# Kernel tuning notes

Hardware: AMD Instinct MI355X
Metric: run time of the kernel (lower is better)

## Reference

```python
import jax, jax.numpy as jnp
import numpy as np

POOLSCALE = 4  # HSA: avg-pool kernel/stride = (scale, scale*4)

def _avg_pool(x, kh, kw):
    # kernel == stride and dims divisible -> exact reshape-mean pooling
    B, C, H, W = x.shape
    return x.reshape(B, C, H // kh, kh, W // kw, kw).mean(axis=(3, 5))

def setup_inputs() -> dict:
    key = jax.random.key(0)
    k1, k2, k3 = jax.random.split(key, 3)
    shape = (4, 64, 192, 192)
    return {
        "K": jax.random.normal(k1, shape, dtype=jnp.float32),
        "Q": jax.random.normal(k2, shape, dtype=jnp.float32),
        "V": jax.random.normal(k3, shape, dtype=jnp.float32),
    }

def reference(K, Q, V):
    B, C, H, W = Q.shape
    kh, kw = POOLSCALE, POOLSCALE * 4
    Qp = Q.reshape(B, C, H * W).transpose(0, 2, 1)          # [B, HW, C]
    Kp = _avg_pool(K, kh, kw)                               # [B, C, h, w]
    Kp = Kp.reshape(B, C, -1)                               # [B, C, hw_p]
    Vp = _avg_pool(V, kh, kw).reshape(B, C, -1)             # [B, C, hw_p]
    scores = jnp.einsum('bnc,bcm->bnm', Qp, Kp)             # [B, HW, hw_p]
    attn = jax.nn.softmax(scores, axis=1)                   # softmax over query dim (dim=1), as in torch code
    out = jnp.einsum('bcm,bnm->bcn', Vp, attn)              # V_pie @ attn^T -> [B, C, HW]
    return out.reshape(B, C, H, W)
```

## Files before the change

kernel.cpp:

```cpp
#include <hip/hip_runtime.h>
#include <stdint.h>

#define BB 4
#define CC 64
#define HH 192
#define WW 192
#define HWN (HH*WW)
#define KH 4
#define KW 16
#define PW (WW/KW)
#define MP ((HH/KH)*(WW/KW))
#define MITER (MP/64)
#define NCHUNK (HWN/256)
#define SCALE_W 65536.0f
#define INV_SCALE (1.0f/65536.0f)

typedef _Float16 half8 __attribute__((ext_vector_type(8)));
typedef _Float16 half4 __attribute__((ext_vector_type(4)));
typedef float floatx4 __attribute__((ext_vector_type(4)));

static __device__ __forceinline__ void gload16(const void* g, void* l) {
  __builtin_amdgcn_global_load_lds((const __attribute__((address_space(1))) void*)g,
                                   (__attribute__((address_space(3))) void*)l, 16, 0, 0);
}
#define WAITCNT_VM(N) asm volatile("s_waitcnt vmcnt(" #N ")" ::: "memory")
#define WAITCNT_LGKM0 asm volatile("s_waitcnt lgkmcnt(0)" ::: "memory")


__global__ __launch_bounds__(256) void pool_kernel(
    const float* __restrict__ Kin, const float* __restrict__ Vin,
    _Float16* __restrict__ kptF, float* __restrict__ vp) {
  int t = blockIdx.x * 256 + threadIdx.x;
  const int total = BB * CC * MP;
  bool isV = t >= total;
  int idx = isV ? t - total : t;
  int m = idx % MP;
  int c = (idx / MP) % CC;
  int b = idx / (MP * CC);
  int mh = m / PW, mw = m % PW;
  const float* src = (isV ? Vin : Kin) + (((b * CC + c) * HH + mh * KH) * WW + mw * KW);
  float s = 0.f;
#pragma unroll
  for (int r = 0; r < KH; ++r) {
    const float4* row = (const float4*)(src + r * WW);
#pragma unroll
    for (int j = 0; j < KW / 4; ++j) {
      float4 v = row[j];
      s += v.x + v.y + v.z + v.w;
    }
  }
  s *= (1.0f / (KH * KW));
  if (isV) {
    vp[(b * CC + c) * MP + m] = s;
  } else {
    int mi = m >> 6, mloc = m & 63, l15 = mloc >> 2, mf = mloc & 3;
    int ks = c >> 5, lhi = (c >> 3) & 3, e = c & 7;
    int lane = lhi * 16 + l15;
    kptF[(((((b * MITER + mi) * 4 + mf) * 2 + ks)) * 64 + lane) * 8 + e] = (_Float16)s;
  }
}

__global__ __launch_bounds__(576) void colsum_kernel(
    const float* __restrict__ Q, const _Float16* __restrict__ kptF,
    float* __restrict__ part) {
  int b = blockIdx.y;
  int n0 = blockIdx.x * 256;
  int tid = threadIdx.x;
  int wv = tid / 64;
  int lane = tid & 63;
  int l15 = lane & 15, lhi = lane >> 4;

  const _Float16* kb = kptF + b * MITER * 8 * 512;
  half8 bfr[4][2];
#pragma unroll
  for (int mf = 0; mf < 4; ++mf)
#pragma unroll
    for (int ks = 0; ks < 2; ++ks)
      bfr[mf][ks] = *(const half8*)(kb + ((wv * 4 + mf) * 2 + ks) * 512 + lane * 8);

  const float* Qb = Q + b * CC * HWN;
  floatx4 zero = {0.f, 0.f, 0.f, 0.f};
  float s0 = 0.f, s1 = 0.f, s2 = 0.f, s3 = 0.f;

#pragma unroll
  for (int it = 0; it < 8; ++it) {
    int nr = n0 + it * 32 + l15;
    half8 af[2][2];
#pragma unroll
    for (int nf = 0; nf < 2; ++nf)
#pragma unroll
      for (int ks = 0; ks < 2; ++ks)
#pragma unroll
        for (int e = 0; e < 8; ++e)
          af[nf][ks][e] = (_Float16)Qb[(ks * 32 + lhi * 8 + e) * HWN + nr + nf * 16];

    floatx4 sacc[2][4];
#pragma unroll
    for (int nf = 0; nf < 2; ++nf)
#pragma unroll
      for (int mf = 0; mf < 4; ++mf) sacc[nf][mf] = zero;
    __builtin_amdgcn_s_setprio(1);
#pragma unroll
    for (int ks = 0; ks < 2; ++ks)
#pragma unroll
      for (int nf = 0; nf < 2; ++nf)
#pragma unroll
        for (int mf = 0; mf < 4; ++mf)
          sacc[nf][mf] = __builtin_amdgcn_mfma_f32_16x16x32_f16(
              af[nf][ks], bfr[mf][ks], sacc[nf][mf], 0, 0, 0);
    __builtin_amdgcn_s_setprio(0);

#pragma unroll
    for (int nf = 0; nf < 2; ++nf)
#pragma unroll
      for (int r = 0; r < 4; ++r) {
        s0 += __expf(sacc[nf][0][r]);
        s1 += __expf(sacc[nf][1][r]);
        s2 += __expf(sacc[nf][2][r]);
        s3 += __expf(sacc[nf][3][r]);
      }
  }

  s0 += __shfl_xor(s0, 16); s0 += __shfl_xor(s0, 32);
  s1 += __shfl_xor(s1, 16); s1 += __shfl_xor(s1, 32);
  s2 += __shfl_xor(s2, 16); s2 += __shfl_xor(s2, 32);
  s3 += __shfl_xor(s3, 16); s3 += __shfl_xor(s3, 32);
  if (lane < 16) {
    float* p = part + (b * NCHUNK + blockIdx.x) * MP + wv * 64 + l15 * 4;
    p[0] = s0; p[1] = s1; p[2] = s2; p[3] = s3;
  }
}

__global__ __launch_bounds__(256) void colsum_reduce_kernel(
    const float* __restrict__ part, float* __restrict__ colsum) {
  int t = blockIdx.x * 256 + threadIdx.x;
  int m = t % MP;
  int b = t / MP;
  const float* p = part + b * NCHUNK * MP + m;
  float a0 = 0.f, a1 = 0.f, a2 = 0.f, a3 = 0.f;
#pragma unroll 4
  for (int nc = 0; nc < NCHUNK; nc += 4) {
    a0 += p[(nc + 0) * MP];
    a1 += p[(nc + 1) * MP];
    a2 += p[(nc + 2) * MP];
    a3 += p[(nc + 3) * MP];
  }
  colsum[t] = (a0 + a1) + (a2 + a3);
}

__global__ __launch_bounds__(256) void wprep_kernel(
    const float* __restrict__ vp, const float* __restrict__ colsum,
    _Float16* __restrict__ wqF) {
  int t = blockIdx.x * 256 + threadIdx.x;
  int m = t % MP;
  int c = (t / MP) % CC;
  int b = t / (CC * MP);
  float w = vp[t] / colsum[b * MP + m] * SCALE_W;
  int cf = c >> 4, l15 = c & 15;
  int mi = m >> 6, mloc = m & 63;
  int ks = mloc >> 5, lhi = (mloc >> 3) & 3, e = mloc & 7;
  int lane = lhi * 16 + l15;
  wqF[((((b * MITER + mi) * 4 + cf) * 2 + ks) * 64 + lane) * 8 + e] = (_Float16)w;
}

__global__ __launch_bounds__(256, 2) void attn_main_kernel(
    const float* __restrict__ Q, const _Float16* __restrict__ kptF,
    const _Float16* __restrict__ wqF, float* __restrict__ out) {
  __shared__ char lds[3 * 16384 + 4 * 4096];
  char* stg = lds;
  int b = blockIdx.y;
  int n0 = blockIdx.x * 128;
  int tid = threadIdx.x;
  int wv = tid >> 6;
  int lane = tid & 63;
  int l15 = lane & 15, lhi = lane >> 4;
  char* eb = lds + 49152 + wv * 4096;

  const _Float16* kb = kptF + b * MITER * 8 * 512;
  const _Float16* wb = wqF + b * MITER * 8 * 512;

#define STAGE_A(tt, ss)                                                        \
  {                                                                            \
    int q0_ = wv * 4;                                                          \
    _Pragma("unroll") for (int j_ = 0; j_ < 4; ++j_) {                         \
      int q_ = q0_ + j_;                                                       \
      const _Float16* sp_ = (q_ < 8 ? kb + (tt) * 4096 + q_ * 512              \
                                    : wb + (tt) * 4096 + (q_ - 8) * 512) +     \
                            lane * 8;                                          \
      gload16(sp_, stg + (ss) * 16384 + q_ * 1024);                            \
    }                                                                          \
  }

  STAGE_A(0, 0);
  STAGE_A(1, 1);

  const float* Qb = Q + b * CC * HWN;
  int nrow = n0 + wv * 32 + l15;
  half8 afrag[2][2];
#pragma unroll
  for (int nf = 0; nf < 2; ++nf)
#pragma unroll
    for (int ks = 0; ks < 2; ++ks)
#pragma unroll
      for (int e = 0; e < 8; ++e)
        afrag[nf][ks][e] = (_Float16)Qb[(ks * 32 + lhi * 8 + e) * HWN + nrow + nf * 16];

  floatx4 zero = {0.f, 0.f, 0.f, 0.f};
  floatx4 oacc[4][2];
#pragma unroll
  for (int cf = 0; cf < 4; ++cf)
#pragma unroll
    for (int nf = 0; nf < 2; ++nf) oacc[cf][nf] = zero;

  WAITCNT_VM(4);
  __builtin_amdgcn_sched_barrier(0);
  __builtin_amdgcn_s_barrier();

#pragma unroll
  for (int mi = 0; mi < MITER; ++mi) {
    const int sc = mi % 3;
    const int spv = (mi + 2) % 3;

    if (mi >= 1) {
      if (mi <= 7) { WAITCNT_VM(4); } else { WAITCNT_VM(0); }
      __builtin_amdgcn_sched_barrier(0);
      __builtin_amdgcn_s_barrier();
    }

    half8 bfr[4][2];
#pragma unroll
    for (int mf = 0; mf < 4; ++mf)
#pragma unroll
      for (int ks = 0; ks < 2; ++ks)
        bfr[mf][ks] = *(const half8*)(stg + sc * 16384 + (mf * 2 + ks) * 1024 + lane * 16);
    half8 wfr[4][2];
    half8 ef[2][2];
    if (mi >= 1) {
#pragma unroll
      for (int cf = 0; cf < 4; ++cf)
#pragma unroll
        for (int ks = 0; ks < 2; ++ks)
          wfr[cf][ks] = *(const half8*)(stg + spv * 16384 + 8192 + (cf * 2 + ks) * 1024 + lane * 16);
#pragma unroll
      for (int nf = 0; nf < 2; ++nf)
#pragma unroll
        for (int ks = 0; ks < 2; ++ks) {
          int nl = nf * 16 + l15;
          int slot = (ks * 4 + lhi) ^ (nl & 7);
          ef[nf][ks] = *(const half8*)(eb + nl * 128 + (slot << 4));
        }
    }

    WAITCNT_LGKM0;
    __builtin_amdgcn_sched_barrier(0);
    __builtin_amdgcn_s_barrier();

    if (mi + 2 < MITER) STAGE_A(mi + 2, spv);

    floatx4 sacc[2][4];
#pragma unroll
    for (int nf = 0; nf < 2; ++nf)
#pragma unroll
      for (int mf = 0; mf < 4; ++mf) sacc[nf][mf] = zero;
    __builtin_amdgcn_s_setprio(1);
#pragma unroll
    for (int ks = 0; ks < 2; ++ks)
#pragma unroll
      for (int nf = 0; nf < 2; ++nf)
#pragma unroll
        for (int mf = 0; mf < 4; ++mf)
          sacc[nf][mf] = __builtin_amdgcn_mfma_f32_16x16x32_f16(
              afrag[nf][ks], bfr[mf][ks], sacc[nf][mf], 0, 0, 0);
    if (mi >= 1) {
#pragma unroll
      for (int ks = 0; ks < 2; ++ks)
#pragma unroll
        for (int cf = 0; cf < 4; ++cf)
#pragma unroll
          for (int nf = 0; nf < 2; ++nf)
            oacc[cf][nf] = __builtin_amdgcn_mfma_f32_16x16x32_f16(
                wfr[cf][ks], ef[nf][ks], oacc[cf][nf], 0, 0, 0);
    }
    __builtin_amdgcn_s_setprio(0);

#pragma unroll
    for (int nf = 0; nf < 2; ++nf)
#pragma unroll
      for (int r = 0; r < 4; ++r) {
        int nl = nf * 16 + lhi * 4 + r;
        half4 h;
#pragma unroll
        for (int mf = 0; mf < 4; ++mf) h[mf] = (_Float16)__expf(sacc[nf][mf][r]);
        int byte = nl * 128 + ((((l15 >> 1) ^ (nl & 7))) << 4) + ((l15 & 1) << 3);
        *(half4*)(eb + byte) = h;
      }
  }

  {
    half8 wfr[4][2];
#pragma unroll
    for (int cf = 0; cf < 4; ++cf)
#pragma unroll
      for (int ks = 0; ks < 2; ++ks)
        wfr[cf][ks] = *(const half8*)(stg + 2 * 16384 + 8192 + (cf * 2 + ks) * 1024 + lane * 16);
    half8 ef[2][2];
#pragma unroll
    for (int nf = 0; nf < 2; ++nf)
#pragma unroll
      for (int ks = 0; ks < 2; ++ks) {
        int nl = nf * 16 + l15;
        int slot = (ks * 4 + lhi) ^ (nl & 7);
        ef[nf][ks] = *(const half8*)(eb + nl * 128 + (slot << 4));
      }
    __builtin_amdgcn_s_setprio(1);
#pragma unroll
    for (int ks = 0; ks < 2; ++ks)
#pragma unroll
      for (int cf = 0; cf < 4; ++cf)
#pragma unroll
        for (int nf = 0; nf < 2; ++nf)
          oacc[cf][nf] = __builtin_amdgcn_mfma_f32_16x16x32_f16(
              wfr[cf][ks], ef[nf][ks], oacc[cf][nf], 0, 0, 0);
    __builtin_amdgcn_s_setprio(0);
  }

  float* ob = out + b * CC * HWN;
#pragma unroll
  for (int cf = 0; cf < 4; ++cf)
#pragma unroll
    for (int nf = 0; nf < 2; ++nf)
#pragma unroll
      for (int r = 0; r < 4; ++r) {
        int c = cf * 16 + lhi * 4 + r;
        int n = n0 + wv * 32 + nf * 16 + l15;
        ob[c * HWN + n] = oacc[cf][nf][r] * INV_SCALE;
      }
}

extern "C" void kernel_launch(void* const* d_in, const int* in_sizes, int n_in,
                              void* d_out, int out_size, void* d_ws, size_t ws_size,
                              hipStream_t stream) {
  const float* K = (const float*)d_in[0];
  const float* Q = (const float*)d_in[1];
  const float* V = (const float*)d_in[2];
  float* out = (float*)d_out;
  char* ws = (char*)d_ws;
  _Float16* kptF  = (_Float16*)(ws);
  float*    vp    = (float*)(ws + 294912);
  _Float16* wqF   = (_Float16*)(ws + 294912 + 589824);
  float*    colsum = (float*)(ws + 294912 + 589824 + 294912);
  float*    part  = out;

  pool_kernel<<<(2 * BB * CC * MP) / 256, 256, 0, stream>>>(K, V, kptF, vp);
  colsum_kernel<<<dim3(NCHUNK, BB), 576, 0, stream>>>(Q, kptF, part);
  colsum_reduce_kernel<<<(BB * MP) / 256, 256, 0, stream>>>(part, colsum);
  wprep_kernel<<<(BB * CC * MP) / 256, 256, 0, stream>>>(vp, colsum, wqF);
  attn_main_kernel<<<dim3(HWN / 128, BB), 256, 0, stream>>>(Q, kptF, wqF, out);
}
```

Before: 99.23 us.

## Pre-pack Q to fp16 fragments, fold exp in registers, restructure colsum

Adds a qprep kernel that converts Q to fp16 once in MFMA fragment layout, so the colsum and main attention kernels read packed halves instead of gathering strided fp32. The main kernel now computes scores transposed (K·Q) so exp'd scores feed the second MFMA directly from registers, dropping the LDS round trip and per-wave scratch buffer. It also drops to a 2-stage LDS pipeline and uses exp2 with log2e folded into K. Colsum is reorganized into per-64-row units with a two-level reduction. This adds extra launches and a Q fp16 buffer write/read in exchange for less global gather traffic and LDS traffic.

```diff
diff --git a/kernel.cpp b/kernel.cpp
--- a/kernel.cpp
+++ b/kernel.cpp
@@ -11,12 +11,14 @@
 #define PW (WW/KW)
 #define MP ((HH/KH)*(WW/KW))
 #define MITER (MP/64)
-#define NCHUNK (HWN/256)
+#define NBTOT (HWN/32)
+#define NUNIT (HWN/64)
+#define NGRP 36
 #define SCALE_W 65536.0f
 #define INV_SCALE (1.0f/65536.0f)
+#define LOG2E 1.44269504088896f
 
 typedef _Float16 half8 __attribute__((ext_vector_type(8)));
-typedef _Float16 half4 __attribute__((ext_vector_type(4)));
 typedef float floatx4 __attribute__((ext_vector_type(4)));
 
 static __device__ __forceinline__ void gload16(const void* g, void* l) {
@@ -24,7 +26,6 @@
                                    (__attribute__((address_space(3))) void*)l, 16, 0, 0);
 }
 #define WAITCNT_VM(N) asm volatile("s_waitcnt vmcnt(" #N ")" ::: "memory")
-#define WAITCNT_LGKM0 asm volatile("s_waitcnt lgkmcnt(0)" ::: "memory")
 
 
 __global__ __launch_bounds__(256) void pool_kernel(
@@ -53,97 +54,138 @@
   if (isV) {
     vp[(b * CC + c) * MP + m] = s;
   } else {
-    int mi = m >> 6, mloc = m & 63, l15 = mloc >> 2, mf = mloc & 3;
+    int mi = m >> 6, w = m & 63, mf = w >> 4, l15 = w & 15;
     int ks = c >> 5, lhi = (c >> 3) & 3, e = c & 7;
     int lane = lhi * 16 + l15;
-    kptF[(((((b * MITER + mi) * 4 + mf) * 2 + ks)) * 64 + lane) * 8 + e] = (_Float16)s;
-  }
-}
-
-__global__ __launch_bounds__(576) void colsum_kernel(
-    const float* __restrict__ Q, const _Float16* __restrict__ kptF,
+    kptF[((((b * MITER + mi) * 4 + mf) * 2 + ks) * 64 + lane) * 8 + e] =
+        (_Float16)(s * LOG2E);
+  }
+}
+
+__global__ __launch_bounds__(256) void qprep_kernel(
+    const float* __restrict__ Q, _Float16* __restrict__ qF) {
+  int t = blockIdx.x * 256 + threadIdx.x;
+  int chunk = t >> 6;
+  int lane = t & 63;
+  int nf = chunk & 1;
+  int ks = (chunk >> 1) & 1;
+  int idx = chunk >> 2;
+  int nb = idx % NBTOT;
+  int b = idx / NBTOT;
+  int c0 = ks * 32 + (lane >> 4) * 8;
+  int n = nb * 32 + nf * 16 + (lane & 15);
+  const float* Qb = Q + (b * CC + c0) * HWN + n;
+  half8 h;
+#pragma unroll
+  for (int e = 0; e < 8; ++e) h[e] = (_Float16)Qb[e * HWN];
+  *(half8*)(qF + chunk * 512 + lane * 8) = h;
+}
+
+__global__ __launch_bounds__(256) void colsum_qf2_kernel(
+    const _Float16* __restrict__ qF, const _Float16* __restrict__ kptF,
     float* __restrict__ part) {
+  int tid = threadIdx.x;
+  int lane = tid & 63;
+  int l15 = lane & 15;
+  int u = blockIdx.x * 4 + (tid >> 6);
+  int b = u / NUNIT;
+  int un = u % NUNIT;
+
+  const _Float16* qc = qF + (size_t)((b * NBTOT + un * 2) * 4) * 512 + lane * 8;
+  half8 af[2][2][2];
+#pragma unroll
+  for (int nb = 0; nb < 2; ++nb)
+#pragma unroll
+    for (int ks = 0; ks < 2; ++ks)
+#pragma unroll
+      for (int nf = 0; nf < 2; ++nf)
+        af[nb][nf][ks] = *(const half8*)(qc + (nb * 4 + ks * 2 + nf) * 512);
+
+  const _Float16* kb = kptF + b * MITER * 8 * 512;
+  floatx4 zero = {0.f, 0.f, 0.f, 0.f};
+  float* pout = part + (size_t)(b * NUNIT + un) * MP;
+
+#pragma unroll
+  for (int mi = 0; mi < MITER; ++mi) {
+    half8 bfr[4][2];
+#pragma unroll
+    for (int mf = 0; mf < 4; ++mf)
+#pragma unroll
+      for (int ks = 0; ks < 2; ++ks)
+        bfr[mf][ks] = *(const half8*)(kb + ((mi * 4 + mf) * 2 + ks) * 512 + lane * 8);
+
+    float s0 = 0.f, s1 = 0.f, s2 = 0.f, s3 = 0.f;
+#pragma unroll
+    for (int nb = 0; nb < 2; ++nb) {
+      floatx4 sacc[2][4];
+#pragma unroll
+      for (int nf = 0; nf < 2; ++nf)
+#pragma unroll
+        for (int mf = 0; mf < 4; ++mf) sacc[nf][mf] = zero;
+      __builtin_amdgcn_s_setprio(1);
+#pragma unroll
+      for (int ks = 0; ks < 2; ++ks)
+#pragma unroll
+        for (int nf = 0; nf < 2; ++nf)
+#pragma unroll
+          for (int mf = 0; mf < 4; ++mf)
+            sacc[nf][mf] = __builtin_amdgcn_mfma_f32_16x16x32_f16(
+                af[nb][nf][ks], bfr[mf][ks], sacc[nf][mf], 0, 0, 0);
+      __builtin_amdgcn_s_setprio(0);
+#pragma unroll
+      for (int nf = 0; nf < 2; ++nf)
+#pragma unroll
+        for (int r = 0; r < 4; ++r) {
+          s0 += exp2f(sacc[nf][0][r]);
+          s1 += exp2f(sacc[nf][1][r]);
+          s2 += exp2f(sacc[nf][2][r]);
+          s3 += exp2f(sacc[nf][3][r]);
+        }
+    }
+    s0 += __shfl_xor(s0, 16); s0 += __shfl_xor(s0, 32);
+    s1 += __shfl_xor(s1, 16); s1 += __shfl_xor(s1, 32);
+    s2 += __shfl_xor(s2, 16); s2 += __shfl_xor(s2, 32);
+    s3 += __shfl_xor(s3, 16); s3 += __shfl_xor(s3, 32);
+    if (lane < 16) {
+      float* p = pout + mi * 64;
+      p[0 * 16 + l15] = s0;
+      p[1 * 16 + l15] = s1;
+      p[2 * 16 + l15] = s2;
+      p[3 * 16 + l15] = s3;
+    }
+  }
+}
+
+__global__ __launch_bounds__(576) void colsum_reduceA_kernel(
+    const float* __restrict__ part, float* __restrict__ part2) {
+  int m = threadIdx.x;
+  int g = blockIdx.x;
   int b = blockIdx.y;
-  int n0 = blockIdx.x * 256;
-  int tid = threadIdx.x;
-  int wv = tid / 64;
-  int lane = tid & 63;
-  int l15 = lane & 15, lhi = lane >> 4;
-
-  const _Float16* kb = kptF + b * MITER * 8 * 512;
-  half8 bfr[4][2];
-#pragma unroll
-  for (int mf = 0; mf < 4; ++mf)
-#pragma unroll
-    for (int ks = 0; ks < 2; ++ks)
-      bfr[mf][ks] = *(const half8*)(kb + ((wv * 4 + mf) * 2 + ks) * 512 + lane * 8);
-
-  const float* Qb = Q + b * CC * HWN;
-  floatx4 zero = {0.f, 0.f, 0.f, 0.f};
-  float s0 = 0.f, s1 = 0.f, s2 = 0.f, s3 = 0.f;
-
-#pragma unroll
-  for (int it = 0; it < 8; ++it) {
-    int nr = n0 + it * 32 + l15;
-    half8 af[2][2];
-#pragma unroll
-    for (int nf = 0; nf < 2; ++nf)
-#pragma unroll
-      for (int ks = 0; ks < 2; ++ks)
-#pragma unroll
-        for (int e = 0; e < 8; ++e)
-          af[nf][ks][e] = (_Float16)Qb[(ks * 32 + lhi * 8 + e) * HWN + nr + nf * 16];
-
-    floatx4 sacc[2][4];
-#pragma unroll
-    for (int nf = 0; nf < 2; ++nf)
-#pragma unroll
-      for (int mf = 0; mf < 4; ++mf) sacc[nf][mf] = zero;
-    __builtin_amdgcn_s_setprio(1);
-#pragma unroll
-    for (int ks = 0; ks < 2; ++ks)
-#pragma unroll
-      for (int nf = 0; nf < 2; ++nf)
-#pragma unroll
-        for (int mf = 0; mf < 4; ++mf)
-          sacc[nf][mf] = __builtin_amdgcn_mfma_f32_16x16x32_f16(
-              af[nf][ks], bfr[mf][ks], sacc[nf][mf], 0, 0, 0);
-    __builtin_amdgcn_s_setprio(0);
-
-#pragma unroll
-    for (int nf = 0; nf < 2; ++nf)
-#pragma unroll
-      for (int r = 0; r < 4; ++r) {
-        s0 += __expf(sacc[nf][0][r]);
-        s1 += __expf(sacc[nf][1][r]);
-        s2 += __expf(sacc[nf][2][r]);
-        s3 += __expf(sacc[nf][3][r]);
-      }
-  }
-
-  s0 += __shfl_xor(s0, 16); s0 += __shfl_xor(s0, 32);
-  s1 += __shfl_xor(s1, 16); s1 += __shfl_xor(s1, 32);
-  s2 += __shfl_xor(s2, 16); s2 += __shfl_xor(s2, 32);
-  s3 += __shfl_xor(s3, 16); s3 += __shfl_xor(s3, 32);
-  if (lane < 16) {
-    float* p = part + (b * NCHUNK + blockIdx.x) * MP + wv * 64 + l15 * 4;
-    p[0] = s0; p[1] = s1; p[2] = s2; p[3] = s3;
-  }
-}
-
-__global__ __launch_bounds__(256) void colsum_reduce_kernel(
-    const float* __restrict__ part, float* __restrict__ colsum) {
+  const float* p = part + (size_t)(b * NUNIT + g * 16) * MP + m;
+  float a0 = 0.f, a1 = 0.f, a2 = 0.f, a3 = 0.f;
+#pragma unroll
+  for (int j = 0; j < 16; j += 4) {
+    a0 += p[(size_t)(j + 0) * MP];
+    a1 += p[(size_t)(j + 1) * MP];
+    a2 += p[(size_t)(j + 2) * MP];
+    a3 += p[(size_t)(j + 3) * MP];
+  }
+  part2[(size_t)(b * NGRP + g) * MP + m] = (a0 + a1) + (a2 + a3);
+}
+
+__global__ __launch_bounds__(256) void colsum_reduceB_kernel(
+    const float* __restrict__ part2, float* __restrict__ colsum) {
   int t = blockIdx.x * 256 + threadIdx.x;
   int m = t % MP;
   int b = t / MP;
-  const float* p = part + b * NCHUNK * MP + m;
+  const float* p = part2 + (size_t)b * NGRP * MP + m;
   float a0 = 0.f, a1 = 0.f, a2 = 0.f, a3 = 0.f;
-#pragma unroll 4
-  for (int nc = 0; nc < NCHUNK; nc += 4) {
-    a0 += p[(nc + 0) * MP];
-    a1 += p[(nc + 1) * MP];
-    a2 += p[(nc + 2) * MP];
-    a3 += p[(nc + 3) * MP];
+#pragma unroll
+  for (int g = 0; g < NGRP; g += 4) {
+    a0 += p[(size_t)(g + 0) * MP];
+    a1 += p[(size_t)(g + 1) * MP];
+    a2 += p[(size_t)(g + 2) * MP];
+    a3 += p[(size_t)(g + 3) * MP];
   }
   colsum[t] = (a0 + a1) + (a2 + a3);
 }
@@ -157,29 +199,28 @@
   int b = t / (CC * MP);
   float w = vp[t] / colsum[b * MP + m] * SCALE_W;
   int cf = c >> 4, l15 = c & 15;
-  int mi = m >> 6, mloc = m & 63;
-  int ks = mloc >> 5, lhi = (mloc >> 3) & 3, e = mloc & 7;
+  int mi = m >> 6, wl = m & 63;
+  int ks = wl >> 5, v = wl & 31;
+  int lhi = (v & 15) >> 2;
+  int e = (v >> 4) * 4 + (v & 3);
   int lane = lhi * 16 + l15;
   wqF[((((b * MITER + mi) * 4 + cf) * 2 + ks) * 64 + lane) * 8 + e] = (_Float16)w;
 }
 
-__global__ __launch_bounds__(256, 2) void attn_main_kernel(
-    const float* __restrict__ Q, const _Float16* __restrict__ kptF,
+__global__ __launch_bounds__(256) void attn_v3_kernel(
+    const _Float16* __restrict__ qF, const _Float16* __restrict__ kptF,
     const _Float16* __restrict__ wqF, float* __restrict__ out) {
-  __shared__ char lds[3 * 16384 + 4 * 4096];
-  char* stg = lds;
+  __shared__ char stg[2 * 16384];
   int b = blockIdx.y;
-  int n0 = blockIdx.x * 128;
   int tid = threadIdx.x;
   int wv = tid >> 6;
   int lane = tid & 63;
   int l15 = lane & 15, lhi = lane >> 4;
-  char* eb = lds + 49152 + wv * 4096;
 
   const _Float16* kb = kptF + b * MITER * 8 * 512;
   const _Float16* wb = wqF + b * MITER * 8 * 512;
 
-#define STAGE_A(tt, ss)                                                        \
+#define STAGE_V3(tt, ss)                                                       \
   {                                                                            \
     int q0_ = wv * 4;                                                          \
     _Pragma("unroll") for (int j_ = 0; j_ < 4; ++j_) {                         \
@@ -191,19 +232,16 @@
     }                                                                          \
   }
 
-  STAGE_A(0, 0);
-  STAGE_A(1, 1);
-
-  const float* Qb = Q + b * CC * HWN;
-  int nrow = n0 + wv * 32 + l15;
+  STAGE_V3(0, 0);
+
+  int nb = blockIdx.x * 4 + wv;
+  const _Float16* qc = qF + (size_t)((b * NBTOT + nb) * 4) * 512 + lane * 8;
   half8 afrag[2][2];
 #pragma unroll
-  for (int nf = 0; nf < 2; ++nf)
-#pragma unroll
-    for (int ks = 0; ks < 2; ++ks)
-#pragma unroll
-      for (int e = 0; e < 8; ++e)
-        afrag[nf][ks][e] = (_Float16)Qb[(ks * 32 + lhi * 8 + e) * HWN + nrow + nf * 16];
+  for (int ks = 0; ks < 2; ++ks)
+#pragma unroll
+    for (int nf = 0; nf < 2; ++nf)
+      afrag[nf][ks] = *(const half8*)(qc + (ks * 2 + nf) * 512);
 
   floatx4 zero = {0.f, 0.f, 0.f, 0.f};
   floatx4 oacc[4][2];
@@ -212,20 +250,13 @@
 #pragma unroll
     for (int nf = 0; nf < 2; ++nf) oacc[cf][nf] = zero;
 
-  WAITCNT_VM(4);
-  __builtin_amdgcn_sched_barrier(0);
-  __builtin_amdgcn_s_barrier();
-
 #pragma unroll
   for (int mi = 0; mi < MITER; ++mi) {
-    const int sc = mi % 3;
-    const int spv = (mi + 2) % 3;
-
-    if (mi >= 1) {
-      if (mi <= 7) { WAITCNT_VM(4); } else { WAITCNT_VM(0); }
-      __builtin_amdgcn_sched_barrier(0);
-      __builtin_amdgcn_s_barrier();
-    }
+    const int sc = mi & 1;
+    WAITCNT_VM(0);
+    __builtin_amdgcn_sched_barrier(0);
+    __builtin_amdgcn_s_barrier();
+    if (mi + 1 < MITER) STAGE_V3(mi + 1, sc ^ 1);
 
     half8 bfr[4][2];
 #pragma unroll
@@ -234,94 +265,45 @@
       for (int ks = 0; ks < 2; ++ks)
         bfr[mf][ks] = *(const half8*)(stg + sc * 16384 + (mf * 2 + ks) * 1024 + lane * 16);
     half8 wfr[4][2];
-    half8 ef[2][2];
-    if (mi >= 1) {
-#pragma unroll
-      for (int cf = 0; cf < 4; ++cf)
-#pragma unroll
-        for (int ks = 0; ks < 2; ++ks)
-          wfr[cf][ks] = *(const half8*)(stg + spv * 16384 + 8192 + (cf * 2 + ks) * 1024 + lane * 16);
+#pragma unroll
+    for (int cf = 0; cf < 4; ++cf)
+#pragma unroll
+      for (int ks = 0; ks < 2; ++ks)
+        wfr[cf][ks] = *(const half8*)(stg + sc * 16384 + 8192 + (cf * 2 + ks) * 1024 + lane * 16);
+
+    floatx4 sacc[4][2];
+#pragma unroll
+    for (int mf = 0; mf < 4; ++mf)
+#pragma unroll
+      for (int nf = 0; nf < 2; ++nf) sacc[mf][nf] = zero;
+    __builtin_amdgcn_s_setprio(1);
+#pragma unroll
+    for (int ks = 0; ks < 2; ++ks)
+#pragma unroll
+      for (int mf = 0; mf < 4; ++mf)
+#pragma unroll
+        for (int nf = 0; nf < 2; ++nf)
+          sacc[mf][nf] = __builtin_amdgcn_mfma_f32_16x16x32_f16(
+              bfr[mf][ks], afrag[nf][ks], sacc[mf][nf], 0, 0, 0);
+    __builtin_amdgcn_s_setprio(0);
+
+#pragma unroll
+    for (int ks = 0; ks < 2; ++ks) {
+      half8 ef[2];
 #pragma unroll
       for (int nf = 0; nf < 2; ++nf)
 #pragma unroll
-        for (int ks = 0; ks < 2; ++ks) {
-          int nl = nf * 16 + l15;
-          int slot = (ks * 4 + lhi) ^ (nl & 7);
-          ef[nf][ks] = *(const half8*)(eb + nl * 128 + (slot << 4));
-        }
-    }
-
-    WAITCNT_LGKM0;
-    __builtin_amdgcn_sched_barrier(0);
-    __builtin_amdgcn_s_barrier();
-
-    if (mi + 2 < MITER) STAGE_A(mi + 2, spv);
-
-    floatx4 sacc[2][4];
-#pragma unroll
-    for (int nf = 0; nf < 2; ++nf)
-#pragma unroll
-      for (int mf = 0; mf < 4; ++mf) sacc[nf][mf] = zero;
-    __builtin_amdgcn_s_setprio(1);
-#pragma unroll
-    for (int ks = 0; ks < 2; ++ks)
-#pragma unroll
-      for (int nf = 0; nf < 2; ++nf)
-#pragma unroll
-        for (int mf = 0; mf < 4; ++mf)
-          sacc[nf][mf] = __builtin_amdgcn_mfma_f32_16x16x32_f16(
-              afrag[nf][ks], bfr[mf][ks], sacc[nf][mf], 0, 0, 0);
-    if (mi >= 1) {
-#pragma unroll
-      for (int ks = 0; ks < 2; ++ks)
-#pragma unroll
-        for (int cf = 0; cf < 4; ++cf)
-#pragma unroll
-          for (int nf = 0; nf < 2; ++nf)
-            oacc[cf][nf] = __builtin_amdgcn_mfma_f32_16x16x32_f16(
-                wfr[cf][ks], ef[nf][ks], oacc[cf][nf], 0, 0, 0);
-    }
-    __builtin_amdgcn_s_setprio(0);
-
-#pragma unroll
-    for (int nf = 0; nf < 2; ++nf)
-#pragma unroll
-      for (int r = 0; r < 4; ++r) {
-        int nl = nf * 16 + lhi * 4 + r;
-        half4 h;
-#pragma unroll
-        for (int mf = 0; mf < 4; ++mf) h[mf] = (_Float16)__expf(sacc[nf][mf][r]);
-        int byte = nl * 128 + ((((l15 >> 1) ^ (nl & 7))) << 4) + ((l15 & 1) << 3);
-        *(half4*)(eb + byte) = h;
-      }
-  }
-
-  {
-    half8 wfr[4][2];
-#pragma unroll
-    for (int cf = 0; cf < 4; ++cf)
-#pragma unroll
-      for (int ks = 0; ks < 2; ++ks)
-        wfr[cf][ks] = *(const half8*)(stg + 2 * 16384 + 8192 + (cf * 2 + ks) * 1024 + lane * 16);
-    half8 ef[2][2];
-#pragma unroll
-    for (int nf = 0; nf < 2; ++nf)
-#pragma unroll
-      for (int ks = 0; ks < 2; ++ks) {
-        int nl = nf * 16 + l15;
-        int slot = (ks * 4 + lhi) ^ (nl & 7);
-        ef[nf][ks] = *(const half8*)(eb + nl * 128 + (slot << 4));
-      }
-    __builtin_amdgcn_s_setprio(1);
-#pragma unroll
-    for (int ks = 0; ks < 2; ++ks)
+        for (int e = 0; e < 8; ++e)
+          ef[nf][e] = (_Float16)exp2f(sacc[2 * ks + (e >> 2)][nf][e & 3]);
+      __builtin_amdgcn_s_setprio(1);
 #pragma unroll
       for (int cf = 0; cf < 4; ++cf)
 #pragma unroll
         for (int nf = 0; nf < 2; ++nf)
           oacc[cf][nf] = __builtin_amdgcn_mfma_f32_16x16x32_f16(
-              wfr[cf][ks], ef[nf][ks], oacc[cf][nf], 0, 0, 0);
-    __builtin_amdgcn_s_setprio(0);
+              wfr[cf][ks], ef[nf], oacc[cf][nf], 0, 0, 0);
+      __builtin_amdgcn_s_setprio(0);
+    }
   }
 
   float* ob = out + b * CC * HWN;
@@ -332,7 +314,7 @@
 #pragma unroll
       for (int r = 0; r < 4; ++r) {
         int c = cf * 16 + lhi * 4 + r;
-        int n = n0 + wv * 32 + nf * 16 + l15;
+        int n = nb * 32 + nf * 16 + l15;
         ob[c * HWN + n] = oacc[cf][nf][r] * INV_SCALE;
       }
 }
@@ -349,11 +331,16 @@
   float*    vp    = (float*)(ws + 294912);
   _Float16* wqF   = (_Float16*)(ws + 294912 + 589824);
   float*    colsum = (float*)(ws + 294912 + 589824 + 294912);
-  float*    part  = out;
+  const size_t QF_OFF = 1204224;
+  _Float16* qF = (_Float16*)(ws + QF_OFF);
+  float* part  = out;
+  float* part2 = out + 2097152;
 
   pool_kernel<<<(2 * BB * CC * MP) / 256, 256, 0, stream>>>(K, V, kptF, vp);
-  colsum_kernel<<<dim3(NCHUNK, BB), 576, 0, stream>>>(Q, kptF, part);
-  colsum_reduce_kernel<<<(BB * MP) / 256, 256, 0, stream>>>(part, colsum);
+  qprep_kernel<<<(BB * NBTOT * 4 * 64) / 256, 256, 0, stream>>>(Q, qF);
+  colsum_qf2_kernel<<<(BB * NUNIT) / 4, 256, 0, stream>>>(qF, kptF, part);
+  colsum_reduceA_kernel<<<dim3(NGRP, BB), 576, 0, stream>>>(part, part2);
+  colsum_reduceB_kernel<<<(BB * MP) / 256, 256, 0, stream>>>(part2, colsum);
   wprep_kernel<<<(BB * CC * MP) / 256, 256, 0, stream>>>(vp, colsum, wqF);
-  attn_main_kernel<<<dim3(HWN / 128, BB), 256, 0, stream>>>(Q, kptF, wqF, out);
-}
+  attn_v3_kernel<<<dim3(NBTOT / 4, BB), 256, 0, stream>>>(qF, kptF, wqF, out);
+}
```

Result: no change. 100.4 us (+1.2%).
